# Kernel tuning notes

Hardware: AMD Instinct MI355X
Metric: run time of the kernel (lower is better)

The kernel has to match this reference:

```python
import jax, jax.numpy as jnp
import numpy as np

N_NODES = 50000

def _gat_layer(x, src, dst, W, a_l, a_r, bias, alpha, agg, act, n_nodes):
    # x: [N, in]; W: [in, H*F]; a_l, a_r: [H, F]; bias: [H*F]
    H, F = a_l.shape
    z = (x @ W).reshape(n_nodes, H, F)                      # [N,H,F]
    el = jnp.einsum('nhf,hf->nh', z, a_l)                   # [N,H]
    er = jnp.einsum('nhf,hf->nh', z, a_r)                   # [N,H]
    e = jax.nn.leaky_relu(el[src] + er[dst], alpha)         # [E,H]
    # segment softmax over in-edges of each destination node
    m = jax.ops.segment_max(e, dst, num_segments=n_nodes)   # [N,H]
    ex = jnp.exp(e - m[dst])                                # [E,H]
    s = jax.ops.segment_sum(ex, dst, num_segments=n_nodes)  # [N,H]
    attn = ex / jnp.maximum(s[dst], 1e-9)                   # [E,H]
    msg = attn[:, :, None] * z[src]                         # [E,H,F]
    h = jax.ops.segment_sum(msg, dst, num_segments=n_nodes) # [N,H,F]
    # identity residual (in_feats == H*F) as in DGL GATConv
    h = h + x.reshape(n_nodes, -1, F)
    h = h + bias.reshape(1, H, F)
    if agg == 'flatten':
        h = h.reshape(n_nodes, H * F)
    else:  # mean over heads
        h = h.mean(axis=1)
    if act is not None:
        h = act(h)
    return h


def setup_inputs() -> dict:
    key = jax.random.key(0)
    ks = jax.random.split(key, 14)
    N, E, D = N_NODES, 800000, 128
    H, F = 4, 32
    sc_in = 1.0 / np.sqrt(D)
    sc_h = 1.0 / np.sqrt(H * F)
    inp = {
        'feats': jax.random.normal(ks[0], (N, D), jnp.float32),
        'src': jax.random.randint(ks[1], (E,), 0, N),
        'dst': jax.random.randint(ks[2], (E,), 0, N),
        'W1': jax.random.normal(ks[3], (D, H * F), jnp.float32) * sc_in,
        'al1': jax.random.normal(ks[4], (H, F), jnp.float32) * sc_h,
        'ar1': jax.random.normal(ks[5], (H, F), jnp.float32) * sc_h,
        'b1': jnp.zeros((H * F,), jnp.float32),
        'W2': jax.random.normal(ks[6], (H * F, H * F), jnp.float32) * sc_h,
        'al2': jax.random.normal(ks[7], (H, F), jnp.float32) * sc_h,
        'ar2': jax.random.normal(ks[8], (H, F), jnp.float32) * sc_h,
        'b2': jnp.zeros((H * F,), jnp.float32),
        'Wp': jax.random.normal(ks[9], (F, 1), jnp.float32) / np.sqrt(F),
        'bp': jnp.zeros((1,), jnp.float32),
    }
    return inp


def reference(feats, src, dst, W1, al1, ar1, b1, W2, al2, ar2, b2, Wp, bp):
    h = _gat_layer(feats, src, dst, W1, al1, ar1, b1, 0.2, 'flatten', jax.nn.elu, N_NODES)
    h = _gat_layer(h, src, dst, W2, al2, ar2, b2, 0.2, 'mean', None, N_NODES)
    return h @ Wp + bp  # [N, 1]
```

## Files before the change

### kernel.cpp

```cpp
#include <hip/hip_runtime.h>
#include <hip/hip_bf16.h>

#define NN 50000
#define NE 800000
#define HF 128

#define OFF_FLAG   0u
#define OFF_ROWPTR 256u
#define OFF_BSUM   200272u
#define OFF_BOFF   200480u
#define OFF_DEG    200704u
#define OFF_FILL   400896u
#define OFF_ADJ    601088u
#define OFF_FX     3801088u
#define OFF_WC1    16601088u
#define OFF_WC2    16633856u
#define OFF_PAR    16666624u
#define OFF_Z      16668672u
#define OFF_H1     29468672u
#define OFF_EL     42268672u
#define OFF_ER     43068672u

typedef __hip_bfloat16 bf16;
typedef unsigned short us16;

#define N_SMALL 33569

typedef __attribute__((ext_vector_type(8))) short bf16x8;
typedef __attribute__((ext_vector_type(4))) float f32x4;

__device__ __forceinline__ float us2f(us16 u) {
  union { unsigned int i; float f; } c; c.i = ((unsigned int)u) << 16; return c.f;
}
__device__ __forceinline__ us16 f2us(float f) {
  bf16 h = __float2bfloat16(f);
  union { bf16 h; us16 u; } c; c.h = h; return c.u;
}
__device__ __forceinline__ float blo(unsigned v) {
  union { unsigned i; float f; } c; c.i = v << 16; return c.f;
}
__device__ __forceinline__ float bhi(unsigned v) {
  union { unsigned i; float f; } c; c.i = v & 0xffff0000u; return c.f;
}
__device__ __forceinline__ unsigned pk2(float a, float b) {
  return (unsigned)f2us(a) | ((unsigned)f2us(b) << 16);
}

__global__ __launch_bounds__(64) void k_detect(const void* __restrict__ w1raw,
                                               int* __restrict__ flag) {
  const us16* u = (const us16*)w1raw;
  int lane = threadIdx.x;
  int mx = 0;
  for (int i = lane; i < 2048; i += 64) {
    int e = (u[i] >> 7) & 0xFF;
    mx = mx > e ? mx : e;
  }
#pragma unroll
  for (int m = 32; m >= 1; m >>= 1) {
    int o = __shfl_xor(mx, m);
    mx = mx > o ? mx : o;
  }
  if (lane == 0) *flag = (mx >= 135) ? 1 : 0;
}

__global__ __launch_bounds__(256) void k_canon_feats(const void* __restrict__ src,
                                                     us16* __restrict__ dst,
                                                     const int* __restrict__ flag) {
  int i = (blockIdx.x * 256 + threadIdx.x) * 4;
  if (i >= NN * HF) return;
  if (*flag) {
    float4 v = *(const float4*)((const float*)src + i);
    ushort4 o;
    o.x = f2us(v.x); o.y = f2us(v.y); o.z = f2us(v.z); o.w = f2us(v.w);
    *(ushort4*)(dst + i) = o;
  } else {
    *(ushort4*)(dst + i) = *(const ushort4*)((const us16*)src + i);
  }
}

__global__ __launch_bounds__(256) void k_canon_small(
    const void* s0, const void* s1, const void* s2, const void* s3, const void* s4,
    const void* s5, const void* s6, const void* s7, const void* s8, const void* s9,
    us16* d0, us16* d1, us16* d2, us16* d3, us16* d4,
    us16* d5, us16* d6, us16* d7, us16* d8, us16* d9,
    const int* __restrict__ flag) {
  const void* sp[10] = {s0, s1, s2, s3, s4, s5, s6, s7, s8, s9};
  us16* dp[10] = {d0, d1, d2, d3, d4, d5, d6, d7, d8, d9};
  const int cnt[10] = {16384, 16384, 128, 128, 128, 128, 128, 128, 32, 1};
  int f = *flag;
  int gid = blockIdx.x * 256 + threadIdx.x;
  int base = 0;
#pragma unroll
  for (int p = 0; p < 10; ++p) {
    int loc = gid - base;
    if (loc >= 0 && loc < cnt[p])
      dp[p][loc] = f ? f2us(((const float*)sp[p])[loc]) : ((const us16*)sp[p])[loc];
    base += cnt[p];
  }
}

__global__ void k_rank(const int* __restrict__ dst, int* __restrict__ fill,
                       int* __restrict__ rank) {
  int e = blockIdx.x * 256 + threadIdx.x;
  if (e < NE) rank[e] = atomicAdd(&fill[dst[e]], 1);
}

__global__ __launch_bounds__(1024) void k_s1(const int* __restrict__ deg,
                                             int* __restrict__ bsum) {
  __shared__ int red[1024];
  int t = threadIdx.x;
  int i = blockIdx.x * 1024 + t;
  red[t] = (i < NN) ? deg[i] : 0;
  __syncthreads();
  for (int s = 512; s > 0; s >>= 1) {
    if (t < s) red[t] += red[t + s];
    __syncthreads();
  }
  if (t == 0) bsum[blockIdx.x] = red[0];
}

__global__ __launch_bounds__(64) void k_s2(const int* __restrict__ bsum,
                                           int* __restrict__ boff,
                                           int* __restrict__ rowptr) {
  int lane = threadIdx.x;
  const int NB = (NN + 1023) / 1024;
  int v = (lane < NB) ? bsum[lane] : 0;
  int orig = v;
#pragma unroll
  for (int off = 1; off < 64; off <<= 1) {
    int u = __shfl_up(v, off);
    if (lane >= off) v += u;
  }
  if (lane < NB) boff[lane] = v - orig;
  if (lane == 0) rowptr[NN] = NE;
}

__global__ __launch_bounds__(1024) void k_s3(const int* __restrict__ deg,
                                             const int* __restrict__ boff,
                                             int* __restrict__ rowptr) {
  __shared__ int part[1024];
  int t = threadIdx.x;
  int i = blockIdx.x * 1024 + t;
  int d = (i < NN) ? deg[i] : 0;
  part[t] = d;
  __syncthreads();
  for (int off = 1; off < 1024; off <<= 1) {
    int v = (t >= off) ? part[t - off] : 0;
    __syncthreads();
    part[t] += v;
    __syncthreads();
  }
  if (i < NN) rowptr[i] = boff[blockIdx.x] + part[t] - d;
}

__global__ void k_place(const int* __restrict__ src, const int* __restrict__ dst,
                        const int* __restrict__ rowptr, const int* __restrict__ rank,
                        int* __restrict__ adj) {
  int e = blockIdx.x * 256 + threadIdx.x;
  if (e < NE) adj[rowptr[dst[e]] + rank[e]] = src[e];
}

__global__ __launch_bounds__(256) void k_gemm(const us16* __restrict__ X,
                                              const us16* __restrict__ W,
                                              us16* __restrict__ Z) {
  __shared__ us16 Wl[HF * HF];
  int tid = threadIdx.x;
  for (int e = tid; e < HF * HF; e += 256) {
    int k = e >> 7, n = e & 127;
    int d = ((((k >> 5) * 8 + (n >> 4)) * 4 + ((k >> 3) & 3)) * 16 + (n & 15)) * 8 + (k & 7);
    Wl[d] = W[e];
  }
  __syncthreads();

  int w = tid >> 6;
  int lane = tid & 63;
  int q = lane >> 4;
  int c = lane & 15;
  int m0 = blockIdx.x * 64 + w * 16;

  int rA = m0 + c;
  if (rA >= NN) rA = NN - 1;
  const us16* xrow = X + (size_t)rA * HF;

  f32x4 acc[8] = {};
#pragma unroll
  for (int s = 0; s < 4; ++s) {
    bf16x8 a = *(const bf16x8*)&xrow[s * 32 + q * 8];
#pragma unroll
    for (int t = 0; t < 8; ++t) {
      bf16x8 b = *(const bf16x8*)&Wl[((((s * 8) + t) * 4 + q) * 16 + c) * 8];
      acc[t] = __builtin_amdgcn_mfma_f32_16x16x32_bf16(a, b, acc[t], 0, 0, 0);
    }
  }

#pragma unroll
  for (int reg = 0; reg < 4; ++reg) {
    int row = m0 + q * 4 + reg;
    if (row < NN) {
      us16* zrow = Z + (size_t)row * HF;
#pragma unroll
      for (int t = 0; t < 8; ++t) zrow[t * 16 + c] = f2us(acc[t][reg]);
    }
  }
}

__global__ __launch_bounds__(256) void k_coef(const us16* __restrict__ Z,
                                              const us16* __restrict__ al,
                                              const us16* __restrict__ ar,
                                              float* __restrict__ el,
                                              float* __restrict__ er) {
  int t = threadIdx.x;
  int n = blockIdx.x * 2 + (t >> 7);
  int c = t & 127;
  float v = us2f(Z[(size_t)n * HF + c]);
  float pl = v * us2f(al[c]);
  float pr = v * us2f(ar[c]);
#pragma unroll
  for (int m = 16; m >= 1; m >>= 1) {
    pl += __shfl_xor(pl, m);
    pr += __shfl_xor(pr, m);
  }
  if ((c & 31) == 0) {
    int h = c >> 5;
    el[n * 4 + h] = pl;
    er[n * 4 + h] = pr;
  }
}

template <int LAYER>
__global__ __launch_bounds__(256) void k_agg(
    const us16* __restrict__ Z, const float* __restrict__ el,
    const float* __restrict__ er, const int* __restrict__ rowptr,
    const int* __restrict__ adj, const us16* __restrict__ resid,
    const us16* __restrict__ bias, us16* __restrict__ Hout,
    const us16* __restrict__ Wp, const us16* __restrict__ bp,
    void* __restrict__ out, const int* __restrict__ flag) {
  int n = blockIdx.x * 4 + (threadIdx.x >> 6);
  int lane = threadIdx.x & 63;
  int g = lane >> 4;
  int p = lane & 15;
  int hl = p >> 2;
  int f0 = p * 8;
  int begin = rowptr[n];
  int deg = rowptr[n + 1] - begin;
  float erh = er[n * 4 + hl];

  float acc[8] = {};
  float ssum = 0.f;
  for (int i = g; i < deg; i += 4) {
    int s = adj[begin + i];
    float sc = el[s * 4 + hl] + erh;
    sc = sc > 0.f ? sc : 0.2f * sc;
    float ex = __expf(sc);
    ssum += ex;
    uint4 zq = *(const uint4*)&Z[(size_t)s * HF + f0];
    acc[0] = fmaf(ex, blo(zq.x), acc[0]);
    acc[1] = fmaf(ex, bhi(zq.x), acc[1]);
    acc[2] = fmaf(ex, blo(zq.y), acc[2]);
    acc[3] = fmaf(ex, bhi(zq.y), acc[3]);
    acc[4] = fmaf(ex, blo(zq.z), acc[4]);
    acc[5] = fmaf(ex, bhi(zq.z), acc[5]);
    acc[6] = fmaf(ex, blo(zq.w), acc[6]);
    acc[7] = fmaf(ex, bhi(zq.w), acc[7]);
  }
  ssum += __shfl_xor(ssum, 16); ssum += __shfl_xor(ssum, 32);
#pragma unroll
  for (int j = 0; j < 8; ++j) {
    acc[j] += __shfl_xor(acc[j], 16);
    acc[j] += __shfl_xor(acc[j], 32);
  }
  float inv = 1.f / fmaxf(ssum, 1e-9f);

  uint4 xq = *(const uint4*)&resid[(size_t)n * HF + f0];
  uint4 bq = *(const uint4*)&bias[f0];
  float t0 = fmaf(acc[0], inv, blo(xq.x) + blo(bq.x));
  float t1 = fmaf(acc[1], inv, bhi(xq.x) + bhi(bq.x));
  float t2 = fmaf(acc[2], inv, blo(xq.y) + blo(bq.y));
  float t3 = fmaf(acc[3], inv, bhi(xq.y) + bhi(bq.y));
  float t4 = fmaf(acc[4], inv, blo(xq.z) + blo(bq.z));
  float t5 = fmaf(acc[5], inv, bhi(xq.z) + bhi(bq.z));
  float t6 = fmaf(acc[6], inv, blo(xq.w) + blo(bq.w));
  float t7 = fmaf(acc[7], inv, bhi(xq.w) + bhi(bq.w));

  if (LAYER == 1) {
    t0 = t0 > 0.f ? t0 : __expf(t0) - 1.f;
    t1 = t1 > 0.f ? t1 : __expf(t1) - 1.f;
    t2 = t2 > 0.f ? t2 : __expf(t2) - 1.f;
    t3 = t3 > 0.f ? t3 : __expf(t3) - 1.f;
    t4 = t4 > 0.f ? t4 : __expf(t4) - 1.f;
    t5 = t5 > 0.f ? t5 : __expf(t5) - 1.f;
    t6 = t6 > 0.f ? t6 : __expf(t6) - 1.f;
    t7 = t7 > 0.f ? t7 : __expf(t7) - 1.f;
    if (g == 0) {
      uint4 o;
      o.x = pk2(t0, t1); o.y = pk2(t2, t3); o.z = pk2(t4, t5); o.w = pk2(t6, t7);
      *(uint4*)&Hout[(size_t)n * HF + f0] = o;
    }
  } else {
    t0 += __shfl_xor(t0, 4); t0 += __shfl_xor(t0, 8);
    t1 += __shfl_xor(t1, 4); t1 += __shfl_xor(t1, 8);
    t2 += __shfl_xor(t2, 4); t2 += __shfl_xor(t2, 8);
    t3 += __shfl_xor(t3, 4); t3 += __shfl_xor(t3, 8);
    t4 += __shfl_xor(t4, 4); t4 += __shfl_xor(t4, 8);
    t5 += __shfl_xor(t5, 4); t5 += __shfl_xor(t5, 8);
    t6 += __shfl_xor(t6, 4); t6 += __shfl_xor(t6, 8);
    t7 += __shfl_xor(t7, 4); t7 += __shfl_xor(t7, 8);
    int fw = (p & 3) * 8;
    float pr = 0.25f * (t0 * us2f(Wp[fw]) + t1 * us2f(Wp[fw + 1]) +
                        t2 * us2f(Wp[fw + 2]) + t3 * us2f(Wp[fw + 3]) +
                        t4 * us2f(Wp[fw + 4]) + t5 * us2f(Wp[fw + 5]) +
                        t6 * us2f(Wp[fw + 6]) + t7 * us2f(Wp[fw + 7]));
    pr += __shfl_xor(pr, 1); pr += __shfl_xor(pr, 2);
    if (lane == 0) {
      float res = pr + us2f(bp[0]);
      if (*flag) ((float*)out)[n] = res;
      else ((us16*)out)[n] = f2us(res);
    }
  }
}

extern "C" void kernel_launch(void* const* d_in, const int* in_sizes, int n_in,
                              void* d_out, int out_size, void* d_ws, size_t ws_size,
                              hipStream_t stream) {
  const int* src = (const int*)d_in[1];
  const int* dst = (const int*)d_in[2];
  char* ws = (char*)d_ws;
  int* flag   = (int*)(ws + OFF_FLAG);
  int* rowptr = (int*)(ws + OFF_ROWPTR);
  int* bsum   = (int*)(ws + OFF_BSUM);
  int* boff   = (int*)(ws + OFF_BOFF);
  int* fill   = (int*)(ws + OFF_FILL);
  int* adj    = (int*)(ws + OFF_ADJ);
  us16* fx    = (us16*)(ws + OFF_FX);
  us16* wc1   = (us16*)(ws + OFF_WC1);
  us16* wc2   = (us16*)(ws + OFF_WC2);
  us16* al1   = (us16*)(ws + OFF_PAR + 0);
  us16* ar1   = (us16*)(ws + OFF_PAR + 256);
  us16* b1    = (us16*)(ws + OFF_PAR + 512);
  us16* al2   = (us16*)(ws + OFF_PAR + 768);
  us16* ar2   = (us16*)(ws + OFF_PAR + 1024);
  us16* b2    = (us16*)(ws + OFF_PAR + 1280);
  us16* wp    = (us16*)(ws + OFF_PAR + 1536);
  us16* bp    = (us16*)(ws + OFF_PAR + 1792);
  us16* z     = (us16*)(ws + OFF_Z);
  us16* h1    = (us16*)(ws + OFF_H1);
  float* el   = (float*)(ws + OFF_EL);
  float* er   = (float*)(ws + OFF_ER);
  int* rank   = (int*)(ws + OFF_Z);

  const int NB = (NN + 1023) / 1024;

  hipMemsetAsync(fill, 0, OFF_ADJ - OFF_FILL, stream);

  hipLaunchKernelGGL(k_detect, dim3(1), dim3(64), 0, stream, d_in[3], flag);
  hipLaunchKernelGGL(k_canon_feats, dim3(6250), dim3(256), 0, stream, d_in[0], fx, flag);
  hipLaunchKernelGGL(k_canon_small, dim3((N_SMALL + 255) / 256), dim3(256), 0, stream,
                     d_in[3], d_in[7], d_in[4], d_in[5], d_in[6],
                     d_in[8], d_in[9], d_in[10], d_in[11], d_in[12],
                     wc1, wc2, al1, ar1, b1, al2, ar2, b2, wp, bp, flag);

  hipLaunchKernelGGL(k_rank, dim3(3125), dim3(256), 0, stream, dst, fill, rank);
  hipLaunchKernelGGL(k_s1, dim3(NB), dim3(1024), 0, stream, fill, bsum);
  hipLaunchKernelGGL(k_s2, dim3(1), dim3(64), 0, stream, bsum, boff, rowptr);
  hipLaunchKernelGGL(k_s3, dim3(NB), dim3(1024), 0, stream, fill, boff, rowptr);
  hipLaunchKernelGGL(k_place, dim3(3125), dim3(256), 0, stream, src, dst, rowptr, rank, adj);

  hipLaunchKernelGGL(k_gemm, dim3((NN + 63) / 64), dim3(256), 0, stream, fx, wc1, z);
  hipLaunchKernelGGL(k_coef, dim3(NN / 2), dim3(256), 0, stream, z, al1, ar1, el, er);
  hipLaunchKernelGGL((k_agg<1>), dim3(NN / 4), dim3(256), 0, stream, z, el, er, rowptr, adj,
                     fx, b1, h1, (us16*)nullptr, (us16*)nullptr, (void*)nullptr, flag);
  hipLaunchKernelGGL(k_gemm, dim3((NN + 63) / 64), dim3(256), 0, stream, h1, wc2, z);
  hipLaunchKernelGGL(k_coef, dim3(NN / 2), dim3(256), 0, stream, z, al2, ar2, el, er);
  hipLaunchKernelGGL((k_agg<2>), dim3(NN / 4), dim3(256), 0, stream, z, el, er, rowptr, adj,
                     h1, b2, (us16*)nullptr, wp, bp, d_out, flag);
}
```

Measured before the change: 288.4 us.

## Fuse attention coefficient computation into GEMM epilogue and unroll aggregation loop

Computes el/er dot products directly from the MFMA accumulators in the GEMM epilogue using cross-lane shuffles, removing the separate k_coef kernel and its re-read of Z. Also unrolls the edge aggregation loop by two so two neighbor gathers are in flight per thread. Risks include extra shuffle and register pressure in the GEMM, and el/er now come from fp32 accumulators instead of bf16-rounded Z, which changes numerics slightly.

```diff
diff --git a/kernel.cpp b/kernel.cpp
--- a/kernel.cpp
+++ b/kernel.cpp
@@ -162,7 +162,11 @@
 
 __global__ __launch_bounds__(256) void k_gemm(const us16* __restrict__ X,
                                               const us16* __restrict__ W,
-                                              us16* __restrict__ Z) {
+                                              us16* __restrict__ Z,
+                                              const us16* __restrict__ al,
+                                              const us16* __restrict__ ar,
+                                              float* __restrict__ el,
+                                              float* __restrict__ er) {
   __shared__ us16 Wl[HF * HF];
   int tid = threadIdx.x;
   for (int e = tid; e < HF * HF; e += 256) {
@@ -202,28 +206,37 @@
       for (int t = 0; t < 8; ++t) zrow[t * 16 + c] = f2us(acc[t][reg]);
     }
   }
-}
-
-__global__ __launch_bounds__(256) void k_coef(const us16* __restrict__ Z,
-                                              const us16* __restrict__ al,
-                                              const us16* __restrict__ ar,
-                                              float* __restrict__ el,
-                                              float* __restrict__ er) {
-  int t = threadIdx.x;
-  int n = blockIdx.x * 2 + (t >> 7);
-  int c = t & 127;
-  float v = us2f(Z[(size_t)n * HF + c]);
-  float pl = v * us2f(al[c]);
-  float pr = v * us2f(ar[c]);
-#pragma unroll
-  for (int m = 16; m >= 1; m >>= 1) {
-    pl += __shfl_xor(pl, m);
-    pr += __shfl_xor(pr, m);
-  }
-  if ((c & 31) == 0) {
-    int h = c >> 5;
-    el[n * 4 + h] = pl;
-    er[n * 4 + h] = pr;
+
+  float alv[8], arv[8];
+#pragma unroll
+  for (int t = 0; t < 8; ++t) {
+    alv[t] = us2f(al[t * 16 + c]);
+    arv[t] = us2f(ar[t * 16 + c]);
+  }
+#pragma unroll
+  for (int reg = 0; reg < 4; ++reg) {
+    int row = m0 + q * 4 + reg;
+    float pl[4], pr[4];
+#pragma unroll
+    for (int h = 0; h < 4; ++h) {
+      pl[h] = acc[2 * h][reg] * alv[2 * h] + acc[2 * h + 1][reg] * alv[2 * h + 1];
+      pr[h] = acc[2 * h][reg] * arv[2 * h] + acc[2 * h + 1][reg] * arv[2 * h + 1];
+    }
+#pragma unroll
+    for (int m = 1; m < 16; m <<= 1) {
+#pragma unroll
+      for (int h = 0; h < 4; ++h) {
+        pl[h] += __shfl_xor(pl[h], m);
+        pr[h] += __shfl_xor(pr[h], m);
+      }
+    }
+    if (row < NN) {
+      int cc = c & 3;
+      float vl = cc == 0 ? pl[0] : cc == 1 ? pl[1] : cc == 2 ? pl[2] : pl[3];
+      float vr = cc == 0 ? pr[0] : cc == 1 ? pr[1] : cc == 2 ? pr[2] : pr[3];
+      if (c < 4) el[row * 4 + cc] = vl;
+      else if (c < 8) er[row * 4 + cc] = vr;
+    }
   }
 }
 
@@ -247,21 +260,39 @@
 
   float acc[8] = {};
   float ssum = 0.f;
-  for (int i = g; i < deg; i += 4) {
+  int i = g;
+  for (; i + 4 < deg; i += 8) {
+    int s0 = adj[begin + i];
+    int s1 = adj[begin + i + 4];
+    float l0 = el[s0 * 4 + hl];
+    float l1 = el[s1 * 4 + hl];
+    uint4 za = *(const uint4*)&Z[(size_t)s0 * HF + f0];
+    uint4 zb = *(const uint4*)&Z[(size_t)s1 * HF + f0];
+    float sc0 = l0 + erh; sc0 = sc0 > 0.f ? sc0 : 0.2f * sc0;
+    float sc1 = l1 + erh; sc1 = sc1 > 0.f ? sc1 : 0.2f * sc1;
+    float ex0 = __expf(sc0);
+    float ex1 = __expf(sc1);
+    ssum += ex0 + ex1;
+    acc[0] = fmaf(ex0, blo(za.x), acc[0]); acc[1] = fmaf(ex0, bhi(za.x), acc[1]);
+    acc[2] = fmaf(ex0, blo(za.y), acc[2]); acc[3] = fmaf(ex0, bhi(za.y), acc[3]);
+    acc[4] = fmaf(ex0, blo(za.z), acc[4]); acc[5] = fmaf(ex0, bhi(za.z), acc[5]);
+    acc[6] = fmaf(ex0, blo(za.w), acc[6]); acc[7] = fmaf(ex0, bhi(za.w), acc[7]);
+    acc[0] = fmaf(ex1, blo(zb.x), acc[0]); acc[1] = fmaf(ex1, bhi(zb.x), acc[1]);
+    acc[2] = fmaf(ex1, blo(zb.y), acc[2]); acc[3] = fmaf(ex1, bhi(zb.y), acc[3]);
+    acc[4] = fmaf(ex1, blo(zb.z), acc[4]); acc[5] = fmaf(ex1, bhi(zb.z), acc[5]);
+    acc[6] = fmaf(ex1, blo(zb.w), acc[6]); acc[7] = fmaf(ex1, bhi(zb.w), acc[7]);
+  }
+  if (i < deg) {
     int s = adj[begin + i];
     float sc = el[s * 4 + hl] + erh;
     sc = sc > 0.f ? sc : 0.2f * sc;
     float ex = __expf(sc);
     ssum += ex;
     uint4 zq = *(const uint4*)&Z[(size_t)s * HF + f0];
-    acc[0] = fmaf(ex, blo(zq.x), acc[0]);
-    acc[1] = fmaf(ex, bhi(zq.x), acc[1]);
-    acc[2] = fmaf(ex, blo(zq.y), acc[2]);
-    acc[3] = fmaf(ex, bhi(zq.y), acc[3]);
-    acc[4] = fmaf(ex, blo(zq.z), acc[4]);
-    acc[5] = fmaf(ex, bhi(zq.z), acc[5]);
-    acc[6] = fmaf(ex, blo(zq.w), acc[6]);
-    acc[7] = fmaf(ex, bhi(zq.w), acc[7]);
+    acc[0] = fmaf(ex, blo(zq.x), acc[0]); acc[1] = fmaf(ex, bhi(zq.x), acc[1]);
+    acc[2] = fmaf(ex, blo(zq.y), acc[2]); acc[3] = fmaf(ex, bhi(zq.y), acc[3]);
+    acc[4] = fmaf(ex, blo(zq.z), acc[4]); acc[5] = fmaf(ex, bhi(zq.z), acc[5]);
+    acc[6] = fmaf(ex, blo(zq.w), acc[6]); acc[7] = fmaf(ex, bhi(zq.w), acc[7]);
   }
   ssum += __shfl_xor(ssum, 16); ssum += __shfl_xor(ssum, 32);
 #pragma unroll
@@ -365,12 +396,12 @@
   hipLaunchKernelGGL(k_s3, dim3(NB), dim3(1024), 0, stream, fill, boff, rowptr);
   hipLaunchKernelGGL(k_place, dim3(3125), dim3(256), 0, stream, src, dst, rowptr, rank, adj);
 
-  hipLaunchKernelGGL(k_gemm, dim3((NN + 63) / 64), dim3(256), 0, stream, fx, wc1, z);
-  hipLaunchKernelGGL(k_coef, dim3(NN / 2), dim3(256), 0, stream, z, al1, ar1, el, er);
+  hipLaunchKernelGGL(k_gemm, dim3((NN + 63) / 64), dim3(256), 0, stream, fx, wc1, z,
+                     al1, ar1, el, er);
   hipLaunchKernelGGL((k_agg<1>), dim3(NN / 4), dim3(256), 0, stream, z, el, er, rowptr, adj,
                      fx, b1, h1, (us16*)nullptr, (us16*)nullptr, (void*)nullptr, flag);
-  hipLaunchKernelGGL(k_gemm, dim3((NN + 63) / 64), dim3(256), 0, stream, h1, wc2, z);
-  hipLaunchKernelGGL(k_coef, dim3(NN / 2), dim3(256), 0, stream, z, al2, ar2, el, er);
+  hipLaunchKernelGGL(k_gemm, dim3((NN + 63) / 64), dim3(256), 0, stream, h1, wc2, z,
+                     al2, ar2, el, er);
   hipLaunchKernelGGL((k_agg<2>), dim3(NN / 4), dim3(256), 0, stream, z, el, er, rowptr, adj,
                      h1, b2, (us16*)nullptr, wp, bp, d_out, flag);
 }
```

New measurement: 264.0 us. 1.09x faster.
